# Optimization experiments

Hardware: AMD Instinct MI355X
Metric: run time of the kernel (lower is better)

## Reference

```python
import jax, jax.numpy as jnp
import numpy as np

B, L, H, E = 4, 2048, 16, 64
S, D = L, E

def setup_inputs() -> dict:
    key = jax.random.key(0)
    kq, kk, kv = jax.random.split(key, 3)
    queries = jax.random.normal(kq, (B, L, H, E), dtype=jnp.float32)
    keys = jax.random.normal(kk, (B, S, H, E), dtype=jnp.float32)
    values = jax.random.normal(kv, (B, S, H, D), dtype=jnp.float32)
    return {"queries": queries, "keys": keys, "values": values}

def reference(queries, keys, values):
    # FullAttention with mask_flag=True, attn_mask=None -> causal mask; dropout p=0 (eval).
    b, l, h, e = queries.shape
    scale = 1.0 / jnp.sqrt(jnp.asarray(e, queries.dtype))
    # scores: [B,H,L,S]
    scores = jnp.einsum('blhe,bshe->bhls', queries, keys)
    causal = jnp.triu(jnp.ones((l, l), dtype=bool), k=1)  # True above diagonal -> masked
    scores = jnp.where(causal[None, None, :, :], -jnp.inf, scores)
    A = jax.nn.softmax(scale * scores, axis=-1)
    V = jnp.einsum('bhls,bshd->blhd', A, values)
    return V
```

## Files before the change

kernel.cpp:

```cpp
#include <hip/hip_runtime.h>
#include <math.h>

#define BB 4
#define LL 2048
#define HH 16
#define EE 64
#define HE (HH*EE)

constexpr int QBLK  = 128;
constexpr int KVBLK = 64;
constexpr int NW    = 8;
constexpr int NQT   = LL / QBLK;
constexpr int LDK   = 72;
constexpr float SCL2E = 0.18033688011112042f;

typedef short short8 __attribute__((ext_vector_type(8)));
typedef float f32x4  __attribute__((ext_vector_type(4)));

#define MFMA(a, b, c) __builtin_amdgcn_mfma_f32_16x16x32_bf16((a), (b), (c), 0, 0, 0)

static __device__ __forceinline__ unsigned short f2bf(float f) {
    unsigned u = __float_as_uint(f);
    return (unsigned short)((u + 0x7FFFu + ((u >> 16) & 1u)) >> 16);
}
static __device__ __forceinline__ float bf2f(unsigned short s) {
    return __uint_as_float(((unsigned)s) << 16);
}

__global__ __launch_bounds__(512, 4)
void attn_mfma(const float* __restrict__ Q, const float* __restrict__ K,
               const float* __restrict__ V, float* __restrict__ O)
{
    __shared__ short KsH[KVBLK * LDK];
    __shared__ short KsL[KVBLK * LDK];
    __shared__ short Vt [EE * LDK];
    __shared__ short Pl [NW * 16 * LDK];

    const int bid = blockIdx.x;
    const int qt  = (NQT - 1) - (bid >> 6);
    const int bh  = bid & 63;
    const int b   = bh >> 4, h = bh & 15;
    const size_t base = (size_t)b * LL * HE + (size_t)h * EE;

    const int tid  = threadIdx.x;
    const int wave = tid >> 6, lane = tid & 63;
    const int g    = lane >> 4, c = lane & 15;

    const int q0 = qt * QBLK + wave * 16;

    short8 qh[2], ql[2];
    {
        const float* qp = Q + base + (size_t)(q0 + c) * HE + 8 * g;
        #pragma unroll
        for (int ec = 0; ec < 2; ++ec) {
            float4 f0 = *(const float4*)(qp + ec * 32);
            float4 f1 = *(const float4*)(qp + ec * 32 + 4);
            float fv[8] = {f0.x, f0.y, f0.z, f0.w, f1.x, f1.y, f1.z, f1.w};
            #pragma unroll
            for (int i = 0; i < 8; ++i) {
                float s = fv[i] * SCL2E;
                unsigned short hb = f2bf(s);
                float rem = s - bf2f(hb);
                qh[ec][i] = (short)hb;
                ql[ec][i] = (short)f2bf(rem);
            }
        }
    }

    f32x4 o[4];
    #pragma unroll
    for (int db = 0; db < 4; ++db)
        #pragma unroll
        for (int j = 0; j < 4; ++j) o[db][j] = 0.0f;
    float m_r[4] = {-INFINITY, -INFINITY, -INFINITY, -INFINITY};
    float l_r[4] = {0.f, 0.f, 0.f, 0.f};

    const int ntile = 2 * qt + 2;
    const int srow = tid >> 3;
    const int scc  = (tid & 7) * 8;

    for (int t = 0; t < ntile; ++t) {
        const int j0 = t * KVBLK;

        __syncthreads();
        {
            const float* kp = K + base + (size_t)(j0 + srow) * HE + scc;
            float4 a0 = *(const float4*)(kp);
            float4 a1 = *(const float4*)(kp + 4);
            float fv[8] = {a0.x, a0.y, a0.z, a0.w, a1.x, a1.y, a1.z, a1.w};
            short8 hv, lv;
            #pragma unroll
            for (int i = 0; i < 8; ++i) {
                unsigned short hb = f2bf(fv[i]);
                hv[i] = (short)hb;
                lv[i] = (short)f2bf(fv[i] - bf2f(hb));
            }
            *(short8*)(&KsH[srow * LDK + scc]) = hv;
            *(short8*)(&KsL[srow * LDK + scc]) = lv;

            const float* vp = V + base + (size_t)(j0 + srow) * HE + scc;
            float4 b0 = *(const float4*)(vp);
            float4 b1 = *(const float4*)(vp + 4);
            float gv[8] = {b0.x, b0.y, b0.z, b0.w, b1.x, b1.y, b1.z, b1.w};
            #pragma unroll
            for (int i = 0; i < 8; ++i) {
                const int d = scc + i;
                const int col = srow ^ (((d >> 3) & 7) << 3);
                Vt[d * LDK + col] = (short)f2bf(gv[i]);
            }
        }
        __syncthreads();

        const int wq_end = q0 + 15;
        if (j0 <= wq_end) {
            const bool diag = (j0 + KVBLK - 1) > q0;

            f32x4 s[4];
            #pragma unroll
            for (int kb = 0; kb < 4; ++kb) {
                f32x4 acc; acc[0]=0.f; acc[1]=0.f; acc[2]=0.f; acc[3]=0.f;
                #pragma unroll
                for (int ec = 0; ec < 2; ++ec) {
                    const int roff = (kb * 16 + c) * LDK + ec * 32 + 8 * g;
                    short8 kh = *(const short8*)(&KsH[roff]);
                    short8 kl = *(const short8*)(&KsL[roff]);
                    acc = MFMA(qh[ec], kh, acc);
                    acc = MFMA(ql[ec], kh, acc);
                    acc = MFMA(qh[ec], kl, acc);
                }
                s[kb] = acc;
            }

            float tm[4];
            #pragma unroll
            for (int r = 0; r < 4; ++r) {
                if (diag) {
                    const int qrow = q0 + 4 * g + r;
                    #pragma unroll
                    for (int kb = 0; kb < 4; ++kb)
                        if (j0 + kb * 16 + c > qrow) s[kb][r] = -INFINITY;
                }
                tm[r] = fmaxf(fmaxf(s[0][r], s[1][r]), fmaxf(s[2][r], s[3][r]));
                #pragma unroll
                for (int xm = 1; xm <= 8; xm <<= 1)
                    tm[r] = fmaxf(tm[r], __shfl_xor(tm[r], xm));
            }

            #pragma unroll
            for (int r = 0; r < 4; ++r) {
                const float nm   = fmaxf(m_r[r], tm[r]);
                const float corr = __builtin_amdgcn_exp2f(m_r[r] - nm);
                m_r[r] = nm;
                l_r[r] *= corr;
                #pragma unroll
                for (int db = 0; db < 4; ++db) o[db][r] *= corr;
                #pragma unroll
                for (int kb = 0; kb < 4; ++kb) {
                    const float p = __builtin_amdgcn_exp2f(s[kb][r] - nm);
                    const unsigned short pb = f2bf(p);
                    l_r[r] += bf2f(pb);
                    Pl[(wave * 16 + 4 * g + r) * LDK + kb * 16 + c] = (short)pb;
                }
            }

            #pragma unroll
            for (int kc = 0; kc < 2; ++kc) {
                short8 pa = *(const short8*)(&Pl[(wave * 16 + c) * LDK + kc * 32 + 8 * g]);
                #pragma unroll
                for (int db = 0; db < 4; ++db) {
                    const int d  = db * 16 + c;
                    const int k0 = (kc * 32 + 8 * g) ^ (((d >> 3) & 7) << 3);
                    short8 vb = *(const short8*)(&Vt[d * LDK + k0]);
                    o[db] = MFMA(pa, vb, o[db]);
                }
            }
        }
    }

    #pragma unroll
    for (int r = 0; r < 4; ++r) {
        float ls = l_r[r];
        #pragma unroll
        for (int xm = 1; xm <= 8; xm <<= 1) ls += __shfl_xor(ls, xm);
        const float inv = 1.0f / ls;
        float* op = O + base + (size_t)(q0 + 4 * g + r) * HE + c;
        #pragma unroll
        for (int db = 0; db < 4; ++db)
            op[db * 16] = o[db][r] * inv;
    }
}

extern "C" void kernel_launch(void* const* d_in, const int* in_sizes, int n_in,
                              void* d_out, int out_size, void* d_ws, size_t ws_size,
                              hipStream_t stream) {
    const float* Q = (const float*)d_in[0];
    const float* K = (const float*)d_in[1];
    const float* V = (const float*)d_in[2];
    float* Out = (float*)d_out;

    dim3 grid(BB * HH * NQT);
    dim3 block(512);
    hipLaunchKernelGGL(attn_mfma, grid, block, 0, stream, Q, K, V, Out);
}
```

Baseline: 244.8 us.

## Drop split-bf16 QK products, defer softmax rescale, raise occupancy and MFMA priority

Replaces the three-MFMA hi/lo split bf16 emulation of the QK^T product with a single bf16 product, which removes the low-part K shared buffer and its conversion work. The online-softmax rescale is now skipped unless the running max grows by more than a threshold. Launch bounds are raised to 8 blocks per CU, and s_setprio brackets are placed around the MFMA sections. The precision drop on the scores may raise error relative to the fp32 reference, and the deferred max lets exponentials exceed 1 by up to 2^8.

```diff
diff --git a/kernel.cpp b/kernel.cpp
--- a/kernel.cpp
+++ b/kernel.cpp
@@ -13,6 +13,7 @@
 constexpr int NQT   = LL / QBLK;
 constexpr int LDK   = 72;
 constexpr float SCL2E = 0.18033688011112042f;
+constexpr float DEFER_THR = 8.0f;
 
 typedef short short8 __attribute__((ext_vector_type(8)));
 typedef float f32x4  __attribute__((ext_vector_type(4)));
@@ -23,18 +24,14 @@
     unsigned u = __float_as_uint(f);
     return (unsigned short)((u + 0x7FFFu + ((u >> 16) & 1u)) >> 16);
 }
-static __device__ __forceinline__ float bf2f(unsigned short s) {
-    return __uint_as_float(((unsigned)s) << 16);
-}
 
-__global__ __launch_bounds__(512, 4)
+__global__ __launch_bounds__(512, 8)
 void attn_mfma(const float* __restrict__ Q, const float* __restrict__ K,
                const float* __restrict__ V, float* __restrict__ O)
 {
-    __shared__ short KsH[KVBLK * LDK];
-    __shared__ short KsL[KVBLK * LDK];
-    __shared__ short Vt [EE * LDK];
-    __shared__ short Pl [NW * 16 * LDK];
+    __shared__ short Ks[KVBLK * LDK];
+    __shared__ short Vt[EE * LDK];
+    __shared__ short Pl[NW * 16 * LDK];
 
     const int bid = blockIdx.x;
     const int qt  = (NQT - 1) - (bid >> 6);
@@ -48,7 +45,7 @@
 
     const int q0 = qt * QBLK + wave * 16;
 
-    short8 qh[2], ql[2];
+    short8 qf[2];
     {
         const float* qp = Q + base + (size_t)(q0 + c) * HE + 8 * g;
         #pragma unroll
@@ -57,13 +54,8 @@
             float4 f1 = *(const float4*)(qp + ec * 32 + 4);
             float fv[8] = {f0.x, f0.y, f0.z, f0.w, f1.x, f1.y, f1.z, f1.w};
             #pragma unroll
-            for (int i = 0; i < 8; ++i) {
-                float s = fv[i] * SCL2E;
-                unsigned short hb = f2bf(s);
-                float rem = s - bf2f(hb);
-                qh[ec][i] = (short)hb;
-                ql[ec][i] = (short)f2bf(rem);
-            }
+            for (int i = 0; i < 8; ++i)
+                qf[ec][i] = (short)f2bf(fv[i] * SCL2E);
         }
     }
 
@@ -88,15 +80,10 @@
             float4 a0 = *(const float4*)(kp);
             float4 a1 = *(const float4*)(kp + 4);
             float fv[8] = {a0.x, a0.y, a0.z, a0.w, a1.x, a1.y, a1.z, a1.w};
-            short8 hv, lv;
+            short8 hv;
             #pragma unroll
-            for (int i = 0; i < 8; ++i) {
-                unsigned short hb = f2bf(fv[i]);
-                hv[i] = (short)hb;
-                lv[i] = (short)f2bf(fv[i] - bf2f(hb));
-            }
-            *(short8*)(&KsH[srow * LDK + scc]) = hv;
-            *(short8*)(&KsL[srow * LDK + scc]) = lv;
+            for (int i = 0; i < 8; ++i) hv[i] = (short)f2bf(fv[i]);
+            *(short8*)(&Ks[srow * LDK + scc]) = hv;
 
             const float* vp = V + base + (size_t)(j0 + srow) * HE + scc;
             float4 b0 = *(const float4*)(vp);
@@ -111,25 +98,22 @@
         }
         __syncthreads();
 
-        const int wq_end = q0 + 15;
-        if (j0 <= wq_end) {
+        if (j0 <= q0 + 15) {
             const bool diag = (j0 + KVBLK - 1) > q0;
 
             f32x4 s[4];
+            __builtin_amdgcn_s_setprio(1);
             #pragma unroll
             for (int kb = 0; kb < 4; ++kb) {
                 f32x4 acc; acc[0]=0.f; acc[1]=0.f; acc[2]=0.f; acc[3]=0.f;
-                #pragma unroll
-                for (int ec = 0; ec < 2; ++ec) {
-                    const int roff = (kb * 16 + c) * LDK + ec * 32 + 8 * g;
-                    short8 kh = *(const short8*)(&KsH[roff]);
-                    short8 kl = *(const short8*)(&KsL[roff]);
-                    acc = MFMA(qh[ec], kh, acc);
-                    acc = MFMA(ql[ec], kh, acc);
-                    acc = MFMA(qh[ec], kl, acc);
-                }
+                const int roff = (kb * 16 + c) * LDK + 8 * g;
+                short8 k0 = *(const short8*)(&Ks[roff]);
+                short8 k1 = *(const short8*)(&Ks[roff + 32]);
+                acc = MFMA(qf[0], k0, acc);
+                acc = MFMA(qf[1], k1, acc);
                 s[kb] = acc;
             }
+            __builtin_amdgcn_s_setprio(0);
 
             float tm[4];
             #pragma unroll
@@ -148,24 +132,26 @@
 
             #pragma unroll
             for (int r = 0; r < 4; ++r) {
-                const float nm   = fmaxf(m_r[r], tm[r]);
-                const float corr = __builtin_amdgcn_exp2f(m_r[r] - nm);
-                m_r[r] = nm;
-                l_r[r] *= corr;
-                #pragma unroll
-                for (int db = 0; db < 4; ++db) o[db][r] *= corr;
+                const float nm = fmaxf(m_r[r], tm[r]);
+                if (nm - m_r[r] > DEFER_THR) {
+                    const float corr = __builtin_amdgcn_exp2f(m_r[r] - nm);
+                    l_r[r] *= corr;
+                    #pragma unroll
+                    for (int db = 0; db < 4; ++db) o[db][r] *= corr;
+                    m_r[r] = nm;
+                }
                 #pragma unroll
                 for (int kb = 0; kb < 4; ++kb) {
-                    const float p = __builtin_amdgcn_exp2f(s[kb][r] - nm);
-                    const unsigned short pb = f2bf(p);
-                    l_r[r] += bf2f(pb);
-                    Pl[(wave * 16 + 4 * g + r) * LDK + kb * 16 + c] = (short)pb;
+                    const float p = __builtin_amdgcn_exp2f(s[kb][r] - m_r[r]);
+                    l_r[r] += p;
+                    Pl[(wave * 16 + 4 * g + r) * LDK + kb * 16 + c] = (short)f2bf(p);
                 }
             }
 
             #pragma unroll
             for (int kc = 0; kc < 2; ++kc) {
                 short8 pa = *(const short8*)(&Pl[(wave * 16 + c) * LDK + kc * 32 + 8 * g]);
+                __builtin_amdgcn_s_setprio(1);
                 #pragma unroll
                 for (int db = 0; db < 4; ++db) {
                     const int d  = db * 16 + c;
@@ -173,6 +159,7 @@
                     short8 vb = *(const short8*)(&Vt[d * LDK + k0]);
                     o[db] = MFMA(pa, vb, o[db]);
                 }
+                __builtin_amdgcn_s_setprio(0);
             }
         }
     }
```

Result: slower. 329.5 us (+34.6%).
